# Kernel tuning notes

Measured on AMD Instinct MI355X. Metric: run time of the kernel, lower is better.

Reference implementation:

```python
import jax, jax.numpy as jnp
import numpy as np

# Static graph dimensions (mirror mat_wann config)
B, IN_DIM, NH, NO = 16384, 512, 128, 256
DENSITY = 0.03


def _build_adjacency():
    """Build the static sparse connectivity matrix.

    mat is [NH + NO, IN_DIM + NH]; entry values: 0 = no edge, 1 = linear edge
    (weight only), 2/3/4 = weight then tanh/relu/sigmoid. Hidden rows only read
    input columns (hidden->hidden block zero), output rows read inputs+hiddens.
    Edge order (for weight assignment) is row-major, as in the torch module.
    """
    rng = np.random.default_rng(0)
    p = DENSITY
    probs = [1.0 - p, p / 4, p / 4, p / 4, p / 4]
    mat_h = rng.choice(5, size=(NH, IN_DIM), p=probs)            # hidden rows (input cols only)
    mat_o = rng.choice(5, size=(NO, IN_DIM + NH), p=probs)       # output rows
    rows_h, cols_h = np.nonzero(mat_h)
    acts_h = mat_h[rows_h, cols_h]
    rows_o, cols_o = np.nonzero(mat_o)
    acts_o = mat_o[rows_o, cols_o]
    return (rows_h.astype(np.int32), cols_h.astype(np.int32), acts_h.astype(np.int32),
            rows_o.astype(np.int32), cols_o.astype(np.int32), acts_o.astype(np.int32))


def setup_inputs() -> dict:
    rows_h, cols_h, acts_h, rows_o, cols_o, acts_o = _build_adjacency()
    key = jax.random.key(0)
    kx, kh, ko = jax.random.split(key, 3)
    x = jax.random.normal(kx, (B, IN_DIM), dtype=jnp.float32)
    # one learned scalar weight per edge (nn.Linear(1,1,bias=False) each)
    wh = jax.random.normal(kh, (rows_h.shape[0],), dtype=jnp.float32) * 0.5
    wo = jax.random.normal(ko, (rows_o.shape[0],), dtype=jnp.float32) * 0.5
    return {
        "x": x, "wh": wh, "wo": wo,
        "rows_h": jnp.asarray(rows_h), "cols_h": jnp.asarray(cols_h), "acts_h": jnp.asarray(acts_h),
        "rows_o": jnp.asarray(rows_o), "cols_o": jnp.asarray(cols_o), "acts_o": jnp.asarray(acts_o),
    }


def _edge_act(z, acts):
    # act id 1 -> identity (weight only); 2 -> tanh; 3 -> relu; 4 -> sigmoid
    return jnp.where(acts == 2, jnp.tanh(z),
           jnp.where(acts == 3, jax.nn.relu(z),
           jnp.where(acts == 4, jax.nn.sigmoid(z), z)))


def reference(x, wh, wo, rows_h, cols_h, acts_h, rows_o, cols_o, acts_o):
    # hidden nodes: per-edge scalar weight + per-edge activation, scatter-add to dest
    zh = _edge_act(x[:, cols_h] * wh, acts_h)                     # [B, Eh]
    H = jnp.zeros((x.shape[0], NH), x.dtype).at[:, rows_h].add(zh)  # [B, NH]
    src = jnp.concatenate([x, H], axis=1)                         # [B, IN+NH]
    zo = _edge_act(src[:, cols_o] * wo, acts_o)                   # [B, Eo]
    out = jnp.zeros((x.shape[0], NO), x.dtype).at[:, rows_o].add(zo)
    return jnp.tanh(out)                                          # output_activation
```

## Files before the change

### kernel.cpp

```cpp
#include <hip/hip_runtime.h>
#include <math.h>

#define BATCH   16384
#define IN_DIM  512
#define NH      128
#define NO      256
#define L2E     1.4426950408889634f

__device__ __forceinline__ float fast_rcp(float x) { return __builtin_amdgcn_rcpf(x); }
__device__ __forceinline__ float fast_exp2(float x) {
#if __has_builtin(__builtin_amdgcn_exp2f)
    return __builtin_amdgcn_exp2f(x);
#else
    return exp2f(x);
#endif
}
__device__ __forceinline__ int rfl(int v) { return __builtin_amdgcn_readfirstlane(v); }
__device__ __forceinline__ int rdl(int v, int l) { return __builtin_amdgcn_readlane(v, l); }

__device__ __forceinline__ float fast_tanh(float z) {
    float ex = fast_exp2(2.f * L2E * z);
    return 1.f - 2.f * fast_rcp(1.f + ex);
}
__device__ __forceinline__ float act_k(int a) {
    return (a == 2) ? (2.f * L2E) : ((a == 4) ? -L2E : 0.f);
}

__device__ __forceinline__ unsigned int f2bf_rne(float f) {
    unsigned int u = __float_as_uint(f);
    return (u + 0x7FFFu + ((u >> 16) & 1u)) >> 16;
}
__device__ __forceinline__ float bf2f(unsigned short h) { return __uint_as_float(((unsigned int)h) << 16); }
__device__ __forceinline__ unsigned short f2bf16s(float f) { return (unsigned short)f2bf_rne(f); }

__device__ __forceinline__ int lower_bound_dev(const int* __restrict__ arr, int n, int v) {
    int lo = 0, hi = n;
    while (lo < hi) { int m = (lo + hi) >> 1; if (arr[m] < v) lo = m + 1; else hi = m; }
    return lo;
}
__device__ __forceinline__ int imin(int a, int b) { return a < b ? a : b; }
__device__ __forceinline__ int imax(int a, int b) { return a > b ? a : b; }

#define FXS     514
#define FHS     65
#define MLDS    99072
#define RSU     128
#define FASTN   60

__global__ __launch_bounds__(512)
void prep_rows(const int* __restrict__ rows_h, const int* __restrict__ cols_h,
               const int* __restrict__ acts_h, const float* __restrict__ wh,
               const int* __restrict__ rows_o, const int* __restrict__ cols_o,
               const int* __restrict__ acts_o, const float* __restrict__ wo,
               int Eh, int Eo, unsigned* __restrict__ rrh, unsigned* __restrict__ rro)
{
    const int lane = (int)(threadIdx.x & 63);
    const int wid  = (int)((blockIdx.x * 512 + threadIdx.x) >> 6);
    if (wid >= NH + NO) return;
    const bool isH = wid < NH;
    const int r = isH ? wid : wid - NH;
    const int*   rows = isH ? rows_h : rows_o;
    const int*   cols = isH ? cols_h : cols_o;
    const int*   acts = isH ? acts_h : acts_o;
    const float* ww   = isH ? wh : wo;
    const int    E    = isH ? Eh : Eo;
    unsigned* rec = (isH ? rrh : rro) + (size_t)r * RSU;

    const int e0 = lower_bound_dev(rows, E, r);
    const int e1 = lower_bound_dev(rows, E, r + 1);
    int n = e1 - e0; if (n > 100) n = 100;
    const unsigned long long lt = (1ull << lane) - 1ull;

    int cnt[8] = {0,0,0,0,0,0,0,0};
    for (int g = 0; g < n; g += 64) {
        int seg = -1;
        if (g + lane < n) {
            int e = e0 + g + lane;
            int a = acts[e];
            int col = cols[e];
            seg = (a - 1) + ((!isH && col >= IN_DIM) ? 4 : 0);
        }
        #pragma unroll
        for (int s = 0; s < 8; ++s) cnt[s] += __popcll(__ballot(seg == s));
    }
    int cntp[8], cum[9]; cum[0] = 0;
    #pragma unroll
    for (int s = 0; s < 8; ++s) { cntp[s] = (cnt[s] + 3) & ~3; cum[s + 1] = cum[s] + cntp[s]; }
    const int np = cum[8];

    int t = 0;
    t += imax(0, imin(cum[1] + cntp[1], FASTN) - imin(cum[1], FASTN));
    t += imax(0, imin(cum[5] + cntp[5], FASTN) - imin(cum[5], FASTN));
    int d4 = (cntp[3] - cnt[3]) + (cntp[7] - cnt[7]);
    float initf = (float)t - 0.5f * (float)d4;

    if (lane == 0) {
        rec[0] = (unsigned)cum[1] | ((unsigned)cum[2] << 8) | ((unsigned)cum[3] << 16) | ((unsigned)cum[4] << 24);
        rec[1] = (unsigned)cum[5] | ((unsigned)cum[6] << 8) | ((unsigned)cum[7] << 16) | ((unsigned)np << 24);
        rec[2] = __float_as_uint(initf);
    }

    int pos[8];
    #pragma unroll
    for (int s = 0; s < 8; ++s) pos[s] = cum[s];
    for (int g = 0; g < n; g += 64) {
        int seg = -1; unsigned payload = 0;
        if (g + lane < n) {
            int e = e0 + g + lane;
            int a = acts[e];
            int col = cols[e];
            bool hs = (!isH && col >= IN_DIM);
            seg = (a - 1) + (hs ? 4 : 0);
            unsigned offv = hs ? (unsigned)(col - IN_DIM) : (unsigned)col;
            float w = ww[e];
            float ws = (a == 2) ? (2.f * L2E) * w : ((a == 4) ? -L2E * w : w);
            unsigned wb = (__float_as_uint(ws) + 0x200u) & 0xFFFFFC00u;
            payload = wb | offv;
        }
        #pragma unroll
        for (int s = 0; s < 8; ++s) {
            unsigned long long m = __ballot(seg == s);
            if (seg == s) {
                int idx = pos[s] + __popcll(m & lt);
                rec[idx < FASTN ? 3 + idx : 64 + (idx - FASTN)] = payload;
            }
            pos[s] += __popcll(m);
        }
    }
    #pragma unroll
    for (int s = 0; s < 8; ++s) {
        int d = cntp[s] - cnt[s];
        if (lane < d) {
            int idx = cum[s] + cnt[s] + lane;
            rec[idx < FASTN ? 3 + idx : 64 + (idx - FASTN)] = 0u;
        }
    }
}

template<int ACT>
__device__ __forceinline__ float app(float acc, float v, float w) {
    if (ACT == 1)      return fmaf(v, w, acc);
    else if (ACT == 2) { float ex = fast_exp2(v * w); return fmaf(-2.f, fast_rcp(1.f + ex), acc); }
    else if (ACT == 3) return acc + fmaxf(v * w, 0.f);
    else               { float ex = fast_exp2(v * w); return acc + fast_rcp(1.f + ex); }
}

template<int ACT, bool HS>
__device__ __forceinline__ void seg_run4(float& a0, float& a1,
                                         const unsigned short* __restrict__ Xl,
                                         const float* __restrict__ Hl,
                                         unsigned hv, int lo, int hi)
{
    #pragma unroll 2
    for (int j = lo; j < hi; j += 4) {
        unsigned s0 = (unsigned)rdl((int)hv, j + 3);
        unsigned s1 = (unsigned)rdl((int)hv, j + 4);
        unsigned s2 = (unsigned)rdl((int)hv, j + 5);
        unsigned s3 = (unsigned)rdl((int)hv, j + 6);
        float v0 = HS ? Hl[(s0 & 1023u) * FHS] : bf2f(Xl[s0 & 1023u]);
        float v1 = HS ? Hl[(s1 & 1023u) * FHS] : bf2f(Xl[s1 & 1023u]);
        float v2 = HS ? Hl[(s2 & 1023u) * FHS] : bf2f(Xl[s2 & 1023u]);
        float v3 = HS ? Hl[(s3 & 1023u) * FHS] : bf2f(Xl[s3 & 1023u]);
        a0 = app<ACT>(a0, v0, __uint_as_float(s0 & 0xFFFFFC00u));
        a1 = app<ACT>(a1, v1, __uint_as_float(s1 & 0xFFFFFC00u));
        a0 = app<ACT>(a0, v2, __uint_as_float(s2 & 0xFFFFFC00u));
        a1 = app<ACT>(a1, v3, __uint_as_float(s3 & 0xFFFFFC00u));
    }
}

template<bool OUT>
__device__ __forceinline__ float row_body(unsigned hv, const unsigned* __restrict__ grow,
                                          const unsigned short* __restrict__ Xl,
                                          const float* __restrict__ Hl, int lane)
{
    const unsigned hx = (unsigned)rdl((int)hv, 0);
    const unsigned hy = (unsigned)rdl((int)hv, 1);
    float a0 = __uint_as_float((unsigned)rdl((int)hv, 2));
    float a1 = 0.f;
    const int c1 = hx & 255, c2 = (hx >> 8) & 255, c3 = (hx >> 16) & 255, c4 = (int)(hx >> 24);
    const int c5 = hy & 255, c6 = (hy >> 8) & 255, c7 = (hy >> 16) & 255, np = (int)(hy >> 24);
    const int m1 = imin(c1, FASTN), m2 = imin(c2, FASTN), m3 = imin(c3, FASTN), m4 = imin(c4, FASTN);
    seg_run4<1,false>(a0, a1, Xl, Hl, hv, 0,  m1);
    seg_run4<2,false>(a0, a1, Xl, Hl, hv, m1, m2);
    seg_run4<3,false>(a0, a1, Xl, Hl, hv, m2, m3);
    seg_run4<4,false>(a0, a1, Xl, Hl, hv, m3, m4);
    if (OUT) {
        const int m5 = imin(c5, FASTN), m6 = imin(c6, FASTN), m7 = imin(c7, FASTN), m8 = imin(np, FASTN);
        seg_run4<1,true>(a0, a1, Xl, Hl, hv, m4, m5);
        seg_run4<2,true>(a0, a1, Xl, Hl, hv, m5, m6);
        seg_run4<3,true>(a0, a1, Xl, Hl, hv, m6, m7);
        seg_run4<4,true>(a0, a1, Xl, Hl, hv, m7, m8);
    }
    if (__builtin_expect(np > FASTN, 0)) {
        unsigned hv2 = grow[64 + lane];
        for (int j = FASTN; j < np; ++j) {
            unsigned sp = (unsigned)rdl((int)hv2, j - FASTN);
            int s = (j < c1) ? 0 : (j < c2) ? 1 : (j < c3) ? 2 : (j < c4) ? 3
                  : (j < c5) ? 4 : (j < c6) ? 5 : (j < c7) ? 6 : 7;
            float w = __uint_as_float(sp & 0xFFFFFC00u);
            unsigned off = sp & 1023u;
            float v = (OUT && s >= 4) ? Hl[off * FHS] : bf2f(Xl[off]);
            int a = (s & 3) + 1;
            if (a == 1) a0 = fmaf(v, w, a0);
            else if (a == 2) { float ex = fast_exp2(v * w); a0 += 1.f - 2.f * fast_rcp(1.f + ex); }
            else if (a == 3) a0 += fmaxf(v * w, 0.f);
            else { float ex = fast_exp2(v * w); a0 += fast_rcp(1.f + ex); }
        }
    }
    return a0 + a1;
}

__global__ __launch_bounds__(1024)
void fused_main(const float* __restrict__ x,
                const unsigned* __restrict__ rrh, const unsigned* __restrict__ rro,
                float* __restrict__ out)
{
    extern __shared__ char lds[];
    unsigned short* X   = (unsigned short*)lds;
    float*          Hf  = (float*)(lds + 65792);
    float*          OBT = (float*)lds;
    const int tid  = (int)threadIdx.x;
    const int lane = tid & 63;
    const int wv   = tid >> 6;
    const int rb   = (int)blockIdx.x * 64;
    const unsigned short* Xl = X + (size_t)lane * FXS;
    const float*          Hl = Hf + lane;

    {
        const float4* xv = (const float4*)(x + (size_t)rb * IN_DIM);
        #pragma unroll
        for (int kk = 0; kk < 8; ++kk) {
            int v = tid + kk * 1024;
            int rr = v >> 7, i = v & 127;
            float4 f = xv[v];
            unsigned int lo = f2bf_rne(f.x) | (f2bf_rne(f.y) << 16);
            unsigned int hi = f2bf_rne(f.z) | (f2bf_rne(f.w) << 16);
            unsigned int* dst = (unsigned int*)&X[rr * FXS + i * 4];
            dst[0] = lo; dst[1] = hi;
        }
    }
    __syncthreads();

    {
        unsigned hv = rrh[(size_t)(wv * 8) * RSU + lane];
        #pragma unroll 1
        for (int q = 0; q < 8; ++q) {
            const int r = wv * 8 + q;
            unsigned hvn = hv;
            if (q < 7) hvn = rrh[(size_t)(r + 1) * RSU + lane];
            float acc = row_body<false>(hv, rrh + (size_t)r * RSU, Xl, Hl, lane);
            Hf[r * FHS + lane] = acc;
            hv = hvn;
        }
    }
    __syncthreads();

    float res[NO / 16];
    {
        unsigned hv = rro[(size_t)(wv * 16) * RSU + lane];
        #pragma unroll 1
        for (int q = 0; q < 16; ++q) {
            const int r = wv * 16 + q;
            unsigned hvn = hv;
            if (q < 15) hvn = rro[(size_t)(r + 1) * RSU + lane];
            res[q] = fast_tanh(row_body<true>(hv, rro + (size_t)r * RSU, Xl, Hl, lane));
            hv = hvn;
        }
    }
    __syncthreads();

    #pragma unroll
    for (int q = 0; q < NO / 16; ++q)
        OBT[(wv * (NO / 16) + q) * FHS + lane] = res[q];
    __syncthreads();
    #pragma unroll
    for (int s = 0; s < 4; ++s) {
        const int b = wv * 4 + s;
        #pragma unroll
        for (int i = 0; i < 4; ++i) {
            const int c = lane + i * 64;
            out[(size_t)(rb + b) * NO + c] = OBT[c * FHS + b];
        }
    }
}

#define FT      1024
#define FBPB    64
#define FHS2    65
#define FOBTS   260
#define FLDS    (99072 + 1544)
__device__ __forceinline__ float edge_act2(float z, int a, float k) {
    float ex = fast_exp2(k * z);
    float rc = fast_rcp(1.f + ex);
    return (a == 2) ? (1.f - 2.f * rc) : ((a == 4) ? rc : ((a == 3) ? fmaxf(z, 0.f) : z));
}
__global__ __launch_bounds__(FT)
void wann_fused(const float* __restrict__ x,
                const int* __restrict__ rows_h, const int* __restrict__ cols_h,
                const int* __restrict__ acts_h, const float* __restrict__ wh,
                const int* __restrict__ rows_o, const int* __restrict__ cols_o,
                const int* __restrict__ acts_o, const float* __restrict__ wo,
                float* __restrict__ out, int Eh, int Eo)
{
    extern __shared__ char lds[];
    unsigned short* X   = (unsigned short*)lds;
    float*          H   = (float*)(lds + 65792);
    float*          OBT = (float*)lds;
    int*            offsH = (int*)(lds + 99072);
    int*            offsO = offsH + (NH + 1);
    const int tid  = threadIdx.x;
    const int lane = tid & 63;
    const int wv   = tid >> 6;
    const int rb   = blockIdx.x * FBPB;
    const int* wh_i = (const int*)wh;
    const int* wo_i = (const int*)wo;
    {
        const float4* xv = (const float4*)(x + (size_t)rb * IN_DIM);
        #pragma unroll
        for (int kk = 0; kk < (FBPB * IN_DIM / 4) / FT; ++kk) {
            int v = tid + kk * FT;
            int r = v >> 7, i = v & 127;
            float4 f = xv[v];
            unsigned int lo = (unsigned int)f2bf16s(f.x) | ((unsigned int)f2bf16s(f.y) << 16);
            unsigned int hi = (unsigned int)f2bf16s(f.z) | ((unsigned int)f2bf16s(f.w) << 16);
            unsigned int* dst = (unsigned int*)&X[r * FXS + i * 4];
            dst[0] = lo; dst[1] = hi;
        }
    }
    if (tid <= NH) offsH[tid] = lower_bound_dev(rows_h, Eh, tid);
    else if (tid <= NH + 1 + NO) offsO[tid - (NH + 1)] = lower_bound_dev(rows_o, Eo, tid - (NH + 1));
    __syncthreads();
    for (int r = wv * (NH / 16); r < (wv + 1) * (NH / 16); ++r) {
        const int e0 = rfl(offsH[r]); const int e1 = rfl(offsH[r + 1]);
        float acc = 0.f;
        #pragma unroll 4
        for (int e = e0; e < e1; ++e) {
            int col = rfl(cols_h[e]); int a = rfl(acts_h[e]);
            float w = __int_as_float(rfl(wh_i[e]));
            acc += edge_act2(bf2f(X[lane * FXS + col]) * w, a, act_k(a));
        }
        H[r * FHS2 + lane] = acc;
    }
    __syncthreads();
    float res[NO / 16];
    #pragma unroll
    for (int rr = 0; rr < NO / 16; ++rr) {
        const int r = wv * (NO / 16) + rr;
        const int e0 = rfl(offsO[r]); const int e1 = rfl(offsO[r + 1]);
        float acc = 0.f;
        #pragma unroll 4
        for (int e = e0; e < e1; ++e) {
            int col = rfl(cols_o[e]); int a = rfl(acts_o[e]);
            float w = __int_as_float(rfl(wo_i[e]));
            float v = (col < IN_DIM) ? bf2f(X[lane * FXS + col]) : H[(col - IN_DIM) * FHS2 + lane];
            acc += edge_act2(v * w, a, act_k(a));
        }
        res[rr] = fast_tanh(acc);
    }
    __syncthreads();
    #pragma unroll
    for (int rr = 0; rr < NO / 16; ++rr)
        OBT[lane * FOBTS + wv * (NO / 16) + rr] = res[rr];
    __syncthreads();
    #pragma unroll
    for (int kk = 0; kk < (FBPB * NO / 4) / FT; ++kk) {
        int v = tid + kk * FT;
        int c4 = v & 63, b = v >> 6;
        float4 o = *(const float4*)&OBT[b * FOBTS + c4 * 4];
        *(float4*)&out[(size_t)(rb + b) * NO + c4 * 4] = o;
    }
}

extern "C" void kernel_launch(void* const* d_in, const int* in_sizes, int n_in,
                              void* d_out, int out_size, void* d_ws, size_t ws_size,
                              hipStream_t stream) {
    const float* x      = (const float*)d_in[0];
    const float* wh     = (const float*)d_in[1];
    const float* wo     = (const float*)d_in[2];
    const int*   rows_h = (const int*)d_in[3];
    const int*   cols_h = (const int*)d_in[4];
    const int*   acts_h = (const int*)d_in[5];
    const int*   rows_o = (const int*)d_in[6];
    const int*   cols_o = (const int*)d_in[7];
    const int*   acts_o = (const int*)d_in[8];
    float*       out    = (float*)d_out;

    const int Eh = in_sizes[1];
    const int Eo = in_sizes[2];

    char*     ws  = (char*)d_ws;
    unsigned* rrh = (unsigned*)ws;
    unsigned* rro = (unsigned*)(ws + (size_t)NH * RSU * 4);
    size_t need = (size_t)(NH + NO) * RSU * 4;

    if (ws_size >= need) {
        prep_rows<<<(NH + NO) * 64 / 512, 512, 0, stream>>>(
            rows_h, cols_h, acts_h, wh, rows_o, cols_o, acts_o, wo,
            Eh, Eo, rrh, rro);
        fused_main<<<BATCH / 64, 1024, MLDS, stream>>>(x, rrh, rro, out);
    } else {
        wann_fused<<<BATCH / FBPB, FT, FLDS, stream>>>(
            x, rows_h, cols_h, acts_h, wh, rows_o, cols_o, acts_o, wo, out, Eh, Eo);
    }
}
```

Measured before the change: 152.6 us.

## Replace zero-padded edge groups with mixed-activation tail segment and preload row records

The preprocessing now stores each activation segment rounded down to a multiple of four. Leftover edges go into a per-source tail segment that encodes the activation id in the payload bits, replacing zero-weight padding that still ran exp/rcp work. The main kernel handles the tail with a mixed-activation loop and takes a slow scalar path when the row overflows the fast region. It also preloads all 24 per-wave row record registers before the first barrier and fully unrolls the row loops. That overlaps the global loads with X staging, at the cost of more registers, some weight mantissa bits in tail entries, and branchy tail code.

```diff
diff --git a/kernel.cpp b/kernel.cpp
--- a/kernel.cpp
+++ b/kernel.cpp
@@ -38,8 +38,6 @@
     while (lo < hi) { int m = (lo + hi) >> 1; if (arr[m] < v) lo = m + 1; else hi = m; }
     return lo;
 }
-__device__ __forceinline__ int imin(int a, int b) { return a < b ? a : b; }
-__device__ __forceinline__ int imax(int a, int b) { return a > b ? a : b; }
 
 #define FXS     514
 #define FHS     65
@@ -67,8 +65,8 @@
     unsigned* rec = (isH ? rrh : rro) + (size_t)r * RSU;
 
     const int e0 = lower_bound_dev(rows, E, r);
-    const int e1 = lower_bound_dev(rows, E, r + 1);
-    int n = e1 - e0; if (n > 100) n = 100;
+    const int e1e = lower_bound_dev(rows, E, r + 1);
+    int n = e1e - e0; if (n > 100) n = 100;
     const unsigned long long lt = (1ull << lane) - 1ull;
 
     int cnt[8] = {0,0,0,0,0,0,0,0};
@@ -83,56 +81,54 @@
         #pragma unroll
         for (int s = 0; s < 8; ++s) cnt[s] += __popcll(__ballot(seg == s));
     }
-    int cntp[8], cum[9]; cum[0] = 0;
-    #pragma unroll
-    for (int s = 0; s < 8; ++s) { cntp[s] = (cnt[s] + 3) & ~3; cum[s + 1] = cum[s] + cntp[s]; }
-    const int np = cum[8];
-
-    int t = 0;
-    t += imax(0, imin(cum[1] + cntp[1], FASTN) - imin(cum[1], FASTN));
-    t += imax(0, imin(cum[5] + cntp[5], FASTN) - imin(cum[5], FASTN));
-    int d4 = (cntp[3] - cnt[3]) + (cntp[7] - cnt[7]);
-    float initf = (float)t - 0.5f * (float)d4;
+    int fl[8], tl[8];
+    #pragma unroll
+    for (int s = 0; s < 8; ++s) { fl[s] = cnt[s] & ~3; tl[s] = cnt[s] - fl[s]; }
+    int e_[11];
+    e_[0] = 0;
+    e_[1] = fl[0]; e_[2] = e_[1] + fl[1]; e_[3] = e_[2] + fl[2]; e_[4] = e_[3] + fl[3];
+    e_[5] = e_[4] + tl[0] + tl[1] + tl[2] + tl[3];
+    e_[6] = e_[5] + fl[4]; e_[7] = e_[6] + fl[5]; e_[8] = e_[7] + fl[6]; e_[9] = e_[8] + fl[7];
+    e_[10] = e_[9] + tl[4] + tl[5] + tl[6] + tl[7];
+
+    int fbase[8] = { e_[0], e_[1], e_[2], e_[3], e_[5], e_[6], e_[7], e_[8] };
+    int tbase[8];
+    tbase[0] = e_[4]; tbase[1] = tbase[0] + tl[0]; tbase[2] = tbase[1] + tl[1]; tbase[3] = tbase[2] + tl[2];
+    tbase[4] = e_[9]; tbase[5] = tbase[4] + tl[4]; tbase[6] = tbase[5] + tl[5]; tbase[7] = tbase[6] + tl[6];
 
     if (lane == 0) {
-        rec[0] = (unsigned)cum[1] | ((unsigned)cum[2] << 8) | ((unsigned)cum[3] << 16) | ((unsigned)cum[4] << 24);
-        rec[1] = (unsigned)cum[5] | ((unsigned)cum[6] << 8) | ((unsigned)cum[7] << 16) | ((unsigned)np << 24);
-        rec[2] = __float_as_uint(initf);
-    }
-
-    int pos[8];
-    #pragma unroll
-    for (int s = 0; s < 8; ++s) pos[s] = cum[s];
+        rec[0] = (unsigned)e_[1] | ((unsigned)e_[2] << 8) | ((unsigned)e_[3] << 16) | ((unsigned)e_[4] << 24);
+        rec[1] = (unsigned)e_[5] | ((unsigned)e_[6] << 8) | ((unsigned)e_[7] << 16) | ((unsigned)e_[8] << 24);
+        rec[2] = (unsigned)e_[9] | ((unsigned)e_[10] << 8);
+    }
+
+    int pos[8] = {0,0,0,0,0,0,0,0};
     for (int g = 0; g < n; g += 64) {
-        int seg = -1; unsigned payload = 0;
+        int seg = -1, a = 0; unsigned offv = 0, wbits = 0;
         if (g + lane < n) {
             int e = e0 + g + lane;
-            int a = acts[e];
+            a = acts[e];
             int col = cols[e];
             bool hs = (!isH && col >= IN_DIM);
             seg = (a - 1) + (hs ? 4 : 0);
-            unsigned offv = hs ? (unsigned)(col - IN_DIM) : (unsigned)col;
+            offv = hs ? (unsigned)(col - IN_DIM) : (unsigned)col;
             float w = ww[e];
             float ws = (a == 2) ? (2.f * L2E) * w : ((a == 4) ? -L2E * w : w);
-            unsigned wb = (__float_as_uint(ws) + 0x200u) & 0xFFFFFC00u;
-            payload = wb | offv;
+            wbits = __float_as_uint(ws);
         }
         #pragma unroll
         for (int s = 0; s < 8; ++s) {
             unsigned long long m = __ballot(seg == s);
             if (seg == s) {
-                int idx = pos[s] + __popcll(m & lt);
+                int k = pos[s] + __popcll(m & lt);
+                bool isFloor = (k < fl[s]);
+                int idx = isFloor ? (fbase[s] + k) : (tbase[s] + (k - fl[s]));
+                unsigned payload = isFloor
+                    ? (((wbits + 0x200u) & 0xFFFFFC00u) | offv)
+                    : (((wbits + 0x800u) & 0xFFFFF000u) | ((unsigned)(a - 1) << 10) | offv);
                 rec[idx < FASTN ? 3 + idx : 64 + (idx - FASTN)] = payload;
             }
             pos[s] += __popcll(m);
-        }
-    }
-    #pragma unroll
-    for (int s = 0; s < 8; ++s) {
-        int d = cntp[s] - cnt[s];
-        if (lane < d) {
-            int idx = cum[s] + cnt[s] + lane;
-            rec[idx < FASTN ? 3 + idx : 64 + (idx - FASTN)] = 0u;
         }
     }
 }
@@ -168,46 +164,107 @@
     }
 }
 
+__device__ __forceinline__ float app_mixed(float acc, unsigned p, float v) {
+    int a = (int)((p >> 10) & 3u);
+    float w = __uint_as_float(p & 0xFFFFF000u);
+    float t = v * w;
+    if (a == 0)      acc += t;
+    else if (a == 2) acc += fmaxf(t, 0.f);
+    else {
+        float ex = fast_exp2(t);
+        float rc = fast_rcp(1.f + ex);
+        acc += (a == 1) ? fmaf(-2.f, rc, 1.f) : rc;
+    }
+    return acc;
+}
+
+template<bool HS>
+__device__ __forceinline__ void seg_tail(float& a0, float& a1,
+                                         const unsigned short* __restrict__ Xl,
+                                         const float* __restrict__ Hl,
+                                         unsigned hv, int lo, int hi)
+{
+    int j = lo;
+    for (; j + 3 < hi; j += 4) {
+        unsigned s0 = (unsigned)rdl((int)hv, j + 3);
+        unsigned s1 = (unsigned)rdl((int)hv, j + 4);
+        unsigned s2 = (unsigned)rdl((int)hv, j + 5);
+        unsigned s3 = (unsigned)rdl((int)hv, j + 6);
+        float v0 = HS ? Hl[(s0 & 1023u) * FHS] : bf2f(Xl[s0 & 1023u]);
+        float v1 = HS ? Hl[(s1 & 1023u) * FHS] : bf2f(Xl[s1 & 1023u]);
+        float v2 = HS ? Hl[(s2 & 1023u) * FHS] : bf2f(Xl[s2 & 1023u]);
+        float v3 = HS ? Hl[(s3 & 1023u) * FHS] : bf2f(Xl[s3 & 1023u]);
+        a0 = app_mixed(a0, s0, v0);
+        a1 = app_mixed(a1, s1, v1);
+        a0 = app_mixed(a0, s2, v2);
+        a1 = app_mixed(a1, s3, v3);
+    }
+    if (j + 1 < hi) {
+        unsigned s0 = (unsigned)rdl((int)hv, j + 3);
+        unsigned s1 = (unsigned)rdl((int)hv, j + 4);
+        float v0 = HS ? Hl[(s0 & 1023u) * FHS] : bf2f(Xl[s0 & 1023u]);
+        float v1 = HS ? Hl[(s1 & 1023u) * FHS] : bf2f(Xl[s1 & 1023u]);
+        a0 = app_mixed(a0, s0, v0);
+        a1 = app_mixed(a1, s1, v1);
+        j += 2;
+    }
+    if (j < hi) {
+        unsigned s0 = (unsigned)rdl((int)hv, j + 3);
+        float v0 = HS ? Hl[(s0 & 1023u) * FHS] : bf2f(Xl[s0 & 1023u]);
+        a0 = app_mixed(a0, s0, v0);
+    }
+}
+
 template<bool OUT>
 __device__ __forceinline__ float row_body(unsigned hv, const unsigned* __restrict__ grow,
                                           const unsigned short* __restrict__ Xl,
-                                          const float* __restrict__ Hl, int lane)
+                                          const float* __restrict__ Hl)
 {
     const unsigned hx = (unsigned)rdl((int)hv, 0);
     const unsigned hy = (unsigned)rdl((int)hv, 1);
-    float a0 = __uint_as_float((unsigned)rdl((int)hv, 2));
-    float a1 = 0.f;
-    const int c1 = hx & 255, c2 = (hx >> 8) & 255, c3 = (hx >> 16) & 255, c4 = (int)(hx >> 24);
-    const int c5 = hy & 255, c6 = (hy >> 8) & 255, c7 = (hy >> 16) & 255, np = (int)(hy >> 24);
-    const int m1 = imin(c1, FASTN), m2 = imin(c2, FASTN), m3 = imin(c3, FASTN), m4 = imin(c4, FASTN);
-    seg_run4<1,false>(a0, a1, Xl, Hl, hv, 0,  m1);
-    seg_run4<2,false>(a0, a1, Xl, Hl, hv, m1, m2);
-    seg_run4<3,false>(a0, a1, Xl, Hl, hv, m2, m3);
-    seg_run4<4,false>(a0, a1, Xl, Hl, hv, m3, m4);
-    if (OUT) {
-        const int m5 = imin(c5, FASTN), m6 = imin(c6, FASTN), m7 = imin(c7, FASTN), m8 = imin(np, FASTN);
-        seg_run4<1,true>(a0, a1, Xl, Hl, hv, m4, m5);
-        seg_run4<2,true>(a0, a1, Xl, Hl, hv, m5, m6);
-        seg_run4<3,true>(a0, a1, Xl, Hl, hv, m6, m7);
-        seg_run4<4,true>(a0, a1, Xl, Hl, hv, m7, m8);
-    }
-    if (__builtin_expect(np > FASTN, 0)) {
-        unsigned hv2 = grow[64 + lane];
-        for (int j = FASTN; j < np; ++j) {
-            unsigned sp = (unsigned)rdl((int)hv2, j - FASTN);
-            int s = (j < c1) ? 0 : (j < c2) ? 1 : (j < c3) ? 2 : (j < c4) ? 3
-                  : (j < c5) ? 4 : (j < c6) ? 5 : (j < c7) ? 6 : 7;
-            float w = __uint_as_float(sp & 0xFFFFFC00u);
-            unsigned off = sp & 1023u;
-            float v = (OUT && s >= 4) ? Hl[off * FHS] : bf2f(Xl[off]);
-            int a = (s & 3) + 1;
-            if (a == 1) a0 = fmaf(v, w, a0);
-            else if (a == 2) { float ex = fast_exp2(v * w); a0 += 1.f - 2.f * fast_rcp(1.f + ex); }
-            else if (a == 3) a0 += fmaxf(v * w, 0.f);
-            else { float ex = fast_exp2(v * w); a0 += fast_rcp(1.f + ex); }
-        }
-    }
-    return a0 + a1;
+    const unsigned hz = (unsigned)rdl((int)hv, 2);
+    const int b1 = hx & 255, b2 = (hx >> 8) & 255, b3 = (hx >> 16) & 255, b4 = (int)(hx >> 24);
+    const int b5 = hy & 255, b6 = (hy >> 8) & 255, b7 = (hy >> 16) & 255, b8 = (int)(hy >> 24);
+    const int b9 = hz & 255, b10 = (hz >> 8) & 255;
+    if (__builtin_expect(b10 <= FASTN, 1)) {
+        float a0 = (float)((b2 - b1) + (OUT ? (b7 - b6) : 0));
+        float a1 = 0.f;
+        seg_run4<1,false>(a0, a1, Xl, Hl, hv, 0,  b1);
+        seg_run4<2,false>(a0, a1, Xl, Hl, hv, b1, b2);
+        seg_run4<3,false>(a0, a1, Xl, Hl, hv, b2, b3);
+        seg_run4<4,false>(a0, a1, Xl, Hl, hv, b3, b4);
+        seg_tail<false>(a0, a1, Xl, Hl, hv, b4, b5);
+        if (OUT) {
+            seg_run4<1,true>(a0, a1, Xl, Hl, hv, b5, b6);
+            seg_run4<2,true>(a0, a1, Xl, Hl, hv, b6, b7);
+            seg_run4<3,true>(a0, a1, Xl, Hl, hv, b7, b8);
+            seg_run4<4,true>(a0, a1, Xl, Hl, hv, b8, b9);
+            seg_tail<true>(a0, a1, Xl, Hl, hv, b9, b10);
+        }
+        return a0 + a1;
+    }
+    float a0 = 0.f;
+    for (int j = 0; j < b10; ++j) {
+        unsigned p = (unsigned)rfl((int)grow[j < FASTN ? 3 + j : 64 + (j - FASTN)]);
+        unsigned off = p & 1023u;
+        bool isTailX = (j >= b4 && j < b5);
+        bool isTailH = (j >= b9);
+        bool hsrc = OUT && (j >= b5);
+        float v = hsrc ? Hl[off * FHS] : bf2f(Xl[off]);
+        int a; float w;
+        if (isTailX || isTailH) { a = (int)((p >> 10) & 3u); w = __uint_as_float(p & 0xFFFFF000u); }
+        else {
+            a = (j < b1) ? 0 : (j < b2) ? 1 : (j < b3) ? 2 : (j < b4) ? 3
+              : (j < b6) ? 0 : (j < b7) ? 1 : (j < b8) ? 2 : 3;
+            w = __uint_as_float(p & 0xFFFFFC00u);
+        }
+        float t = v * w;
+        if (a == 0) a0 += t;
+        else if (a == 2) a0 += fmaxf(t, 0.f);
+        else { float ex = fast_exp2(t); float rc = fast_rcp(1.f + ex);
+               a0 += (a == 1) ? (1.f - 2.f * rc) : rc; }
+    }
+    return a0;
 }
 
 __global__ __launch_bounds__(1024)
@@ -239,33 +296,30 @@
             dst[0] = lo; dst[1] = hi;
         }
     }
-    __syncthreads();
-
-    {
-        unsigned hv = rrh[(size_t)(wv * 8) * RSU + lane];
-        #pragma unroll 1
-        for (int q = 0; q < 8; ++q) {
-            const int r = wv * 8 + q;
-            unsigned hvn = hv;
-            if (q < 7) hvn = rrh[(size_t)(r + 1) * RSU + lane];
-            float acc = row_body<false>(hv, rrh + (size_t)r * RSU, Xl, Hl, lane);
-            Hf[r * FHS + lane] = acc;
-            hv = hvn;
-        }
+
+    unsigned hvh[8], hvo[16];
+    #pragma unroll
+    for (int q = 0; q < 8; ++q)
+        hvh[q] = rrh[(size_t)(wv * 8 + q) * RSU + lane];
+    #pragma unroll
+    for (int q = 0; q < 16; ++q)
+        hvo[q] = rro[(size_t)(wv * 16 + q) * RSU + lane];
+
+    __syncthreads();
+
+    #pragma unroll
+    for (int q = 0; q < 8; ++q) {
+        const int r = wv * 8 + q;
+        float acc = row_body<false>(hvh[q], rrh + (size_t)r * RSU, Xl, Hl);
+        Hf[r * FHS + lane] = acc;
     }
     __syncthreads();
 
     float res[NO / 16];
-    {
-        unsigned hv = rro[(size_t)(wv * 16) * RSU + lane];
-        #pragma unroll 1
-        for (int q = 0; q < 16; ++q) {
-            const int r = wv * 16 + q;
-            unsigned hvn = hv;
-            if (q < 15) hvn = rro[(size_t)(r + 1) * RSU + lane];
-            res[q] = fast_tanh(row_body<true>(hv, rro + (size_t)r * RSU, Xl, Hl, lane));
-            hv = hvn;
-        }
+    #pragma unroll
+    for (int q = 0; q < 16; ++q) {
+        const int r = wv * 16 + q;
+        res[q] = fast_tanh(row_body<true>(hvo[q], rro + (size_t)r * RSU, Xl, Hl));
     }
     __syncthreads();
 
```

Result: no change. 149.8 us (-1.8%).
